# Kernel tuning notes

Hardware: AMD Instinct MI355X
Metric: run time of the kernel (lower is better)

Reference implementation:

```python
import jax, jax.numpy as jnp
import numpy as np

TEMPERATURE = 0.07
NEG_INF = -1e9
EPS = 1e-12  # matches F.normalize eps

B, N, D = 512, 128, 512


def _l2norm(x):
    return x / jnp.maximum(jnp.linalg.norm(x, axis=-1, keepdims=True), EPS)


def setup_inputs() -> dict:
    key = jax.random.key(0)
    k1, k2, k3, k4 = jax.random.split(key, 4)
    text_embeddings = jax.random.normal(k1, (B, D), dtype=jnp.float32)
    all_visual_embeddings = jax.random.normal(k2, (B, N, D), dtype=jnp.float32)
    valid = jax.random.bernoulli(k3, 0.9, (B, N))
    gt_indices = jax.random.randint(k4, (B,), 0, N, dtype=jnp.int64 if jax.config.jax_enable_x64 else jnp.int32)
    return {
        'text_embeddings': text_embeddings,
        'all_visual_embeddings': all_visual_embeddings,
        'valid': valid,
        'gt_indices': gt_indices,
    }


def reference(text_embeddings, all_visual_embeddings, valid, gt_indices):
    Bb, Nn, Dd = all_visual_embeddings.shape
    tn = _l2norm(text_embeddings)                 # (B, D)
    vn = _l2norm(all_visual_embeddings)           # (B, N, D)

    gt_c = jnp.clip(gt_indices, 0, Nn - 1)
    barange = jnp.arange(Bb)
    gt_vis = vn[barange, gt_c]                    # (B, D) GT visual per sample
    sample_valid = (gt_indices >= 0) & (gt_indices < Nn) & valid[barange, gt_c]  # (B,)

    pos_sim = jnp.sum(tn * gt_vis, axis=-1) / TEMPERATURE            # (B,)

    # in-sample hard negatives: all valid humans except GT
    sims_in = jnp.einsum('bd,bnd->bn', tn, vn) / TEMPERATURE          # (B, N)
    in_mask = valid & (jnp.arange(Nn)[None, :] != gt_c[:, None])      # (B, N)

    # in-batch negatives: other samples' valid GT visuals
    sims_batch = (tn @ gt_vis.T) / TEMPERATURE                        # (B, B)
    batch_mask = sample_valid[None, :] & ~jnp.eye(Bb, dtype=bool)     # (B, B)

    neg_logits = jnp.concatenate([
        jnp.where(in_mask, sims_in, NEG_INF),
        jnp.where(batch_mask, sims_batch, NEG_INF),
    ], axis=1)                                                        # (B, N+B)

    # CE with label 0 over [pos, negs] = logsumexp - pos
    lse = jax.nn.logsumexp(jnp.concatenate([pos_sim[:, None], neg_logits], axis=1), axis=1)
    loss_per = lse - pos_sim                                          # (B,)

    has_neg = jnp.any(in_mask, axis=1) | jnp.any(batch_mask, axis=1)
    contrib = sample_valid & has_neg
    n_valid = jnp.sum(sample_valid.astype(jnp.float32))
    denom = jnp.maximum(n_valid, 1.0)

    total = jnp.sum(jnp.where(contrib, loss_per, 0.0)) / denom
    max_neg = jnp.max(neg_logits, axis=1)
    correct = contrib & (pos_sim >= max_neg)  # argmax ties go to index 0 (pos)
    accuracy = jnp.sum(correct.astype(jnp.float32)) / denom
    return total, accuracy
```

## Files before the change

kernel.cpp:

```cpp
#include <hip/hip_runtime.h>
#include <hip/hip_bf16.h>
#include <math.h>

constexpr int B_ = 512;
constexpr int N_ = 128;
constexpr int D_ = 512;
constexpr float TEMP_INV = 1.0f / 0.07f;
constexpr float NEG_INF_ = -1e9f;
constexpr float EPS_ = 1e-12f;

constexpr size_t OFF_TN   = 0;
constexpr size_t OFF_GTV  = OFF_TN + (size_t)B_ * D_;
constexpr size_t OFF_POS  = OFF_GTV + (size_t)B_ * D_;
constexpr size_t OFF_LIN  = OFF_POS + B_;
constexpr size_t OFF_LB   = OFF_LIN + (size_t)B_ * N_;
constexpr size_t OFF_SV   = OFF_LB + (size_t)B_ * B_;
constexpr size_t OFF_SCAL = OFF_SV + B_;

__device__ __forceinline__ float wave_sum(float v) {
    for (int off = 32; off; off >>= 1) v += __shfl_xor(v, off);
    return v;
}

__device__ __forceinline__ void detect_flags(const void* raw, int lane, int& f0, int& f1) {
    unsigned int v = ((const unsigned int*)raw)[lane];
    f0 = (__ballot(v == 0x3f800000u) != 0ull) ? 1 : 0;
    f1 = (__ballot((v & 0xffffff00u) != 0u) != 0ull) ? 1 : 0;
}

__device__ __forceinline__ int decode_valid(const void* raw, int f0, int f1, size_t idx) {
    if (f0) return ((const float*)raw)[idx] != 0.0f;
    if (f1) return ((const unsigned char*)raw)[idx] != 0;
    return ((const int*)raw)[idx] != 0;
}

__global__ __launch_bounds__(256) void fused_insample_kernel(
        const float* __restrict__ text,
        const float* __restrict__ visual,
        const int* __restrict__ gt,
        const void* __restrict__ valid_raw,
        float* __restrict__ tn,
        float* __restrict__ gtv,
        float* __restrict__ pos_sim,
        int* __restrict__ svalid,
        float* __restrict__ scal,
        float* __restrict__ lin) {
    int bid = blockIdx.x;
    int b = bid >> 2;
    int tile = bid & 3;
    int tid = threadIdx.x;
    int wave = tid >> 6, lane = tid & 63;

    if (bid == 0 && tid < 3) scal[tid] = 0.0f;

    int f0, f1;
    detect_flags(valid_raw, lane, f0, f1);

    __shared__ float4 tsh4[D_ / 4];
    float* tshf = (float*)tsh4;
    const float* trow = text + (size_t)b * D_;
    float t0 = trow[tid], t1 = trow[tid + 256];
    float sst = wave_sum(t0 * t0 + t1 * t1);
    __shared__ float red[4];
    __shared__ float invt_sh;
    if (lane == 0) red[wave] = sst;
    __syncthreads();
    if (tid == 0) invt_sh = 1.0f / fmaxf(sqrtf(red[0] + red[1] + red[2] + red[3]), EPS_);
    __syncthreads();
    float invt = invt_sh;
    t0 *= invt; t1 *= invt;
    tshf[tid] = t0; tshf[tid + 256] = t1;
    if (tile == 0) {
        tn[(size_t)b * D_ + tid]       = t0;
        tn[(size_t)b * D_ + tid + 256] = t1;
    }
    __syncthreads();

    int g = gt[b];
    int gc = min(max(g, 0), N_ - 1);
    int sub = lane >> 4;
    int s = lane & 15;

    #pragma unroll
    for (int p = 0; p < 2; ++p) {
        int n = tile * 32 + p * 16 + wave * 4 + sub;
        const float4* vrow = (const float4*)(visual + ((size_t)b * N_ + n) * D_);
        float dot = 0.0f, ss = 0.0f;
        #pragma unroll
        for (int it = 0; it < 8; ++it) {
            float4 v = vrow[s + 16 * it];
            float4 t = tsh4[s + 16 * it];
            dot += v.x * t.x + v.y * t.y + v.z * t.z + v.w * t.w;
            ss  += v.x * v.x + v.y * v.y + v.z * v.z + v.w * v.w;
        }
        #pragma unroll
        for (int off = 8; off; off >>= 1) {
            dot += __shfl_xor(dot, off);
            ss  += __shfl_xor(ss, off);
        }
        float inv = 1.0f / fmaxf(sqrtf(ss), EPS_);
        if (s == 0) {
            int vb = decode_valid(valid_raw, f0, f1, (size_t)b * N_ + n);
            bool m = vb && (n != gc);
            lin[(size_t)b * N_ + n] = m ? dot * inv * TEMP_INV : NEG_INF_;
            if (n == gc) {
                pos_sim[b] = dot * inv * TEMP_INV;
                svalid[b] = (g >= 0 && g < N_ && vb) ? 1 : 0;
            }
        }
        if (n == gc) {
            float4* gdst = (float4*)(gtv + (size_t)b * D_);
            #pragma unroll
            for (int it = 0; it < 8; ++it) {
                float4 v = vrow[s + 16 * it];
                gdst[s + 16 * it] = make_float4(v.x * inv, v.y * inv, v.z * inv, v.w * inv);
            }
        }
    }
}

__global__ __launch_bounds__(256) void batch_kernel(const float* __restrict__ gtv,
                                                    const float* __restrict__ tn,
                                                    const int* __restrict__ svalid,
                                                    float* __restrict__ lb) {
    int bid = blockIdx.x;
    int b0 = (bid >> 2) * 4;
    int jbase = (bid & 3) * 128;
    int tid = threadIdx.x;
    __shared__ float4 tsh4[4 * (D_ / 4)];
    #pragma unroll
    for (int idx = tid; idx < 4 * (D_ / 4); idx += 256) {
        int r = idx >> 7, c = idx & 127;
        tsh4[idx] = ((const float4*)tn)[(size_t)(b0 + r) * (D_ / 4) + c];
    }
    __syncthreads();
    int wave = tid >> 6, lane = tid & 63;
    int sub = lane >> 4;
    int s = lane & 15;
    #pragma unroll
    for (int p = 0; p < 8; ++p) {
        int j = jbase + p * 16 + wave * 4 + sub;
        const float4* grow = (const float4*)gtv + (size_t)j * (D_ / 4);
        float a0 = 0.0f, a1 = 0.0f, a2 = 0.0f, a3 = 0.0f;
        #pragma unroll
        for (int it = 0; it < 8; ++it) {
            float4 v  = grow[s + 16 * it];
            float4 t0 = tsh4[0 * 128 + s + 16 * it];
            float4 t1 = tsh4[1 * 128 + s + 16 * it];
            float4 t2 = tsh4[2 * 128 + s + 16 * it];
            float4 t3 = tsh4[3 * 128 + s + 16 * it];
            a0 += v.x * t0.x + v.y * t0.y + v.z * t0.z + v.w * t0.w;
            a1 += v.x * t1.x + v.y * t1.y + v.z * t1.z + v.w * t1.w;
            a2 += v.x * t2.x + v.y * t2.y + v.z * t2.z + v.w * t2.w;
            a3 += v.x * t3.x + v.y * t3.y + v.z * t3.z + v.w * t3.w;
        }
        #pragma unroll
        for (int off = 8; off; off >>= 1) {
            a0 += __shfl_xor(a0, off);
            a1 += __shfl_xor(a1, off);
            a2 += __shfl_xor(a2, off);
            a3 += __shfl_xor(a3, off);
        }
        int sv = svalid[j];
        if (s < 4) {
            float av = (s == 0) ? a0 : (s == 1) ? a1 : (s == 2) ? a2 : a3;
            int brow = b0 + s;
            lb[(size_t)brow * B_ + j] = (sv && j != brow) ? av * TEMP_INV : NEG_INF_;
        }
    }
}

__global__ __launch_bounds__(256) void lse_kernel(const float* __restrict__ logits_in,
                                                  const float* __restrict__ lb,
                                                  const float* __restrict__ pos_sim,
                                                  const int* __restrict__ svalid,
                                                  float* __restrict__ accum,
                                                  int* __restrict__ done,
                                                  float* __restrict__ out) {
    int b = blockIdx.x;
    int tid = threadIdx.x;
    int wave = tid >> 6, lane = tid & 63;
    float pos = pos_sim[b];
    float x0 = (tid < N_) ? logits_in[(size_t)b * N_ + tid]
                          : lb[(size_t)b * B_ + (tid - N_)];
    float x1 = lb[(size_t)b * B_ + (tid + 256 - N_)];
    float x2 = (tid < N_) ? lb[(size_t)b * B_ + (tid + 512 - N_)] : NEG_INF_;
    float lmax = fmaxf(fmaxf(x0, x1), x2);
    for (int off = 32; off; off >>= 1) lmax = fmaxf(lmax, __shfl_xor(lmax, off));
    __shared__ float red[4];
    __shared__ float sh1;
    if (lane == 0) red[wave] = lmax;
    __syncthreads();
    if (tid == 0) sh1 = fmaxf(fmaxf(red[0], red[1]), fmaxf(red[2], red[3]));
    __syncthreads();
    float maxneg = sh1;
    float m = fmaxf(maxneg, pos);
    float lsum = __expf(x0 - m) + __expf(x1 - m) + ((tid < N_) ? __expf(x2 - m) : 0.0f);
    lsum = wave_sum(lsum);
    __syncthreads();
    if (lane == 0) red[wave] = lsum;
    __syncthreads();
    __shared__ int is_last;
    if (tid == 0) {
        float sum = red[0] + red[1] + red[2] + red[3] + __expf(pos - m);
        float lse = m + logf(sum);
        float loss = lse - pos;
        bool has_neg = maxneg > -1e8f;
        bool contrib = (svalid[b] != 0) && has_neg;
        if (contrib) {
            atomicAdd(&accum[0], loss);
            if (pos >= maxneg) atomicAdd(&accum[1], 1.0f);
        }
        __threadfence();
        int prev = atomicAdd(done, 1);
        is_last = (prev == B_ - 1) ? 1 : 0;
    }
    __syncthreads();
    if (is_last) {
        int v = svalid[tid] + svalid[tid + 256];
        for (int off = 32; off; off >>= 1) v += __shfl_xor(v, off);
        __shared__ int ired[4];
        if (lane == 0) ired[wave] = v;
        __syncthreads();
        if (tid == 0) {
            int nv = ired[0] + ired[1] + ired[2] + ired[3];
            float total = atomicAdd(&accum[0], 0.0f);
            float acc   = atomicAdd(&accum[1], 0.0f);
            float denom = fmaxf((float)nv, 1.0f);
            out[0] = total / denom;
            out[1] = acc / denom;
        }
    }
}

extern "C" void kernel_launch(void* const* d_in, const int* in_sizes, int n_in,
                              void* d_out, int out_size, void* d_ws, size_t ws_size,
                              hipStream_t stream) {
    const float* text   = (const float*)d_in[0];
    const float* visual = (const float*)d_in[1];
    const void*  valid  = d_in[2];
    const int*   gt     = (const int*)d_in[3];
    float* out = (float*)d_out;

    float* wsf = (float*)d_ws;
    float* tn      = wsf + OFF_TN;
    float* gtv     = wsf + OFF_GTV;
    float* pos_sim = wsf + OFF_POS;
    float* lin     = wsf + OFF_LIN;
    float* lb      = wsf + OFF_LB;
    int*   svalid  = (int*)(wsf + OFF_SV);
    float* scal    = wsf + OFF_SCAL;
    float* accum   = scal;
    int*   done    = (int*)(scal + 2);

    fused_insample_kernel<<<B_ * 4, 256, 0, stream>>>(text, visual, gt, valid,
                                                      tn, gtv, pos_sim, svalid, scal, lin);
    batch_kernel<<<B_, 256, 0, stream>>>(gtv, tn, svalid, lb);
    lse_kernel<<<B_, 256, 0, stream>>>(lin, lb, pos_sim, svalid, accum, done, out);
}
```

Baseline: 227.4 us.

## Fuse batch-similarity and logsumexp kernels, keep batch logits in shared memory

Merges batch_kernel and lse_kernel into one kernel. Each 512-thread block handles two text rows, computes their 512 in-batch logits into shared memory, then does the logsumexp and accumulation directly. This removes one launch and the round trip of the B×B logits buffer through global memory. The visual loads in the in-sample kernel also become nontemporal loads to reduce cache pollution. The trade-off is that each block now reads all of gtv for only two rows instead of four, which halves reuse of gtv per block and doubles its total reads.

```diff
diff --git a/kernel.cpp b/kernel.cpp
--- a/kernel.cpp
+++ b/kernel.cpp
@@ -1,5 +1,4 @@
 #include <hip/hip_runtime.h>
-#include <hip/hip_bf16.h>
 #include <math.h>
 
 constexpr int B_ = 512;
@@ -9,12 +8,13 @@
 constexpr float NEG_INF_ = -1e9f;
 constexpr float EPS_ = 1e-12f;
 
+typedef float f4v __attribute__((ext_vector_type(4)));
+
 constexpr size_t OFF_TN   = 0;
 constexpr size_t OFF_GTV  = OFF_TN + (size_t)B_ * D_;
 constexpr size_t OFF_POS  = OFF_GTV + (size_t)B_ * D_;
 constexpr size_t OFF_LIN  = OFF_POS + B_;
-constexpr size_t OFF_LB   = OFF_LIN + (size_t)B_ * N_;
-constexpr size_t OFF_SV   = OFF_LB + (size_t)B_ * B_;
+constexpr size_t OFF_SV   = OFF_LIN + (size_t)B_ * N_;
 constexpr size_t OFF_SCAL = OFF_SV + B_;
 
 __device__ __forceinline__ float wave_sum(float v) {
@@ -84,11 +84,11 @@
     #pragma unroll
     for (int p = 0; p < 2; ++p) {
         int n = tile * 32 + p * 16 + wave * 4 + sub;
-        const float4* vrow = (const float4*)(visual + ((size_t)b * N_ + n) * D_);
+        const f4v* vrow = (const f4v*)(visual + ((size_t)b * N_ + n) * D_);
         float dot = 0.0f, ss = 0.0f;
         #pragma unroll
         for (int it = 0; it < 8; ++it) {
-            float4 v = vrow[s + 16 * it];
+            f4v v = __builtin_nontemporal_load(vrow + s + 16 * it);
             float4 t = tsh4[s + 16 * it];
             dot += v.x * t.x + v.y * t.y + v.z * t.z + v.w * t.w;
             ss  += v.x * v.x + v.y * v.y + v.z * v.z + v.w * v.w;
@@ -109,100 +109,88 @@
             }
         }
         if (n == gc) {
-            float4* gdst = (float4*)(gtv + (size_t)b * D_);
+            f4v* gdst = (f4v*)(gtv + (size_t)b * D_);
             #pragma unroll
             for (int it = 0; it < 8; ++it) {
-                float4 v = vrow[s + 16 * it];
-                gdst[s + 16 * it] = make_float4(v.x * inv, v.y * inv, v.z * inv, v.w * inv);
+                f4v v = __builtin_nontemporal_load(vrow + s + 16 * it);
+                gdst[s + 16 * it] = v * inv;
             }
         }
     }
 }
 
-__global__ __launch_bounds__(256) void batch_kernel(const float* __restrict__ gtv,
-                                                    const float* __restrict__ tn,
-                                                    const int* __restrict__ svalid,
-                                                    float* __restrict__ lb) {
-    int bid = blockIdx.x;
-    int b0 = (bid >> 2) * 4;
-    int jbase = (bid & 3) * 128;
+__global__ __launch_bounds__(512) void batch_lse_kernel(
+        const float* __restrict__ gtv,
+        const float* __restrict__ tn,
+        const float* __restrict__ lin,
+        const float* __restrict__ pos_sim,
+        const int* __restrict__ svalid,
+        float* __restrict__ accum,
+        int* __restrict__ done,
+        float* __restrict__ out) {
+    int b0 = blockIdx.x * 2;
     int tid = threadIdx.x;
-    __shared__ float4 tsh4[4 * (D_ / 4)];
-    #pragma unroll
-    for (int idx = tid; idx < 4 * (D_ / 4); idx += 256) {
+    int wave = tid >> 6, lane = tid & 63;
+
+    __shared__ float4 tsh[2 * (D_ / 4)];
+    __shared__ float lbsh[2][B_];
+    for (int idx = tid; idx < 2 * (D_ / 4); idx += 512) {
         int r = idx >> 7, c = idx & 127;
-        tsh4[idx] = ((const float4*)tn)[(size_t)(b0 + r) * (D_ / 4) + c];
-    }
-    __syncthreads();
-    int wave = tid >> 6, lane = tid & 63;
-    int sub = lane >> 4;
-    int s = lane & 15;
-    #pragma unroll
-    for (int p = 0; p < 8; ++p) {
-        int j = jbase + p * 16 + wave * 4 + sub;
+        tsh[idx] = ((const float4*)tn)[(size_t)(b0 + r) * (D_ / 4) + c];
+    }
+    __syncthreads();
+
+    int q = tid >> 4;
+    int s = tid & 15;
+    #pragma unroll 4
+    for (int p = 0; p < 16; ++p) {
+        int j = p * 32 + q;
         const float4* grow = (const float4*)gtv + (size_t)j * (D_ / 4);
-        float a0 = 0.0f, a1 = 0.0f, a2 = 0.0f, a3 = 0.0f;
+        float a0 = 0.0f, a1 = 0.0f;
         #pragma unroll
         for (int it = 0; it < 8; ++it) {
             float4 v  = grow[s + 16 * it];
-            float4 t0 = tsh4[0 * 128 + s + 16 * it];
-            float4 t1 = tsh4[1 * 128 + s + 16 * it];
-            float4 t2 = tsh4[2 * 128 + s + 16 * it];
-            float4 t3 = tsh4[3 * 128 + s + 16 * it];
+            float4 t0 = tsh[0 * 128 + s + 16 * it];
+            float4 t1 = tsh[1 * 128 + s + 16 * it];
             a0 += v.x * t0.x + v.y * t0.y + v.z * t0.z + v.w * t0.w;
             a1 += v.x * t1.x + v.y * t1.y + v.z * t1.z + v.w * t1.w;
-            a2 += v.x * t2.x + v.y * t2.y + v.z * t2.z + v.w * t2.w;
-            a3 += v.x * t3.x + v.y * t3.y + v.z * t3.z + v.w * t3.w;
         }
         #pragma unroll
         for (int off = 8; off; off >>= 1) {
             a0 += __shfl_xor(a0, off);
             a1 += __shfl_xor(a1, off);
-            a2 += __shfl_xor(a2, off);
-            a3 += __shfl_xor(a3, off);
-        }
-        int sv = svalid[j];
-        if (s < 4) {
-            float av = (s == 0) ? a0 : (s == 1) ? a1 : (s == 2) ? a2 : a3;
+        }
+        if (s < 2) {
+            float av = (s == 0) ? a0 : a1;
             int brow = b0 + s;
-            lb[(size_t)brow * B_ + j] = (sv && j != brow) ? av * TEMP_INV : NEG_INF_;
-        }
-    }
-}
-
-__global__ __launch_bounds__(256) void lse_kernel(const float* __restrict__ logits_in,
-                                                  const float* __restrict__ lb,
-                                                  const float* __restrict__ pos_sim,
-                                                  const int* __restrict__ svalid,
-                                                  float* __restrict__ accum,
-                                                  int* __restrict__ done,
-                                                  float* __restrict__ out) {
-    int b = blockIdx.x;
-    int tid = threadIdx.x;
-    int wave = tid >> 6, lane = tid & 63;
+            lbsh[s][j] = (svalid[j] && j != brow) ? av * TEMP_INV : NEG_INF_;
+        }
+    }
+    __syncthreads();
+
+    int r = tid >> 8;
+    int rt = tid & 255;
+    int b = b0 + r;
     float pos = pos_sim[b];
-    float x0 = (tid < N_) ? logits_in[(size_t)b * N_ + tid]
-                          : lb[(size_t)b * B_ + (tid - N_)];
-    float x1 = lb[(size_t)b * B_ + (tid + 256 - N_)];
-    float x2 = (tid < N_) ? lb[(size_t)b * B_ + (tid + 512 - N_)] : NEG_INF_;
+    float x0 = (rt < N_) ? lin[(size_t)b * N_ + rt] : lbsh[r][rt - N_];
+    float x1 = lbsh[r][rt + 256 - N_];
+    float x2 = (rt < N_) ? lbsh[r][rt + 512 - N_] : NEG_INF_;
     float lmax = fmaxf(fmaxf(x0, x1), x2);
     for (int off = 32; off; off >>= 1) lmax = fmaxf(lmax, __shfl_xor(lmax, off));
-    __shared__ float red[4];
-    __shared__ float sh1;
-    if (lane == 0) red[wave] = lmax;
-    __syncthreads();
-    if (tid == 0) sh1 = fmaxf(fmaxf(red[0], red[1]), fmaxf(red[2], red[3]));
-    __syncthreads();
-    float maxneg = sh1;
+    __shared__ float redm[8], reds[8];
+    if (lane == 0) redm[wave] = lmax;
+    __syncthreads();
+    float maxneg = fmaxf(fmaxf(redm[r * 4 + 0], redm[r * 4 + 1]),
+                         fmaxf(redm[r * 4 + 2], redm[r * 4 + 3]));
     float m = fmaxf(maxneg, pos);
-    float lsum = __expf(x0 - m) + __expf(x1 - m) + ((tid < N_) ? __expf(x2 - m) : 0.0f);
+    float lsum = __expf(x0 - m) + __expf(x1 - m) + ((rt < N_) ? __expf(x2 - m) : 0.0f);
     lsum = wave_sum(lsum);
-    __syncthreads();
-    if (lane == 0) red[wave] = lsum;
+    if (lane == 0) reds[wave] = lsum;
     __syncthreads();
     __shared__ int is_last;
-    if (tid == 0) {
-        float sum = red[0] + red[1] + red[2] + red[3] + __expf(pos - m);
+    if (rt == 0) {
+        float sum = reds[r * 4 + 0] + reds[r * 4 + 1] + reds[r * 4 + 2] + reds[r * 4 + 3]
+                  + __expf(pos - m);
         float lse = m + logf(sum);
         float loss = lse - pos;
         bool has_neg = maxneg > -1e8f;
@@ -212,18 +200,23 @@
             if (pos >= maxneg) atomicAdd(&accum[1], 1.0f);
         }
         __threadfence();
+    }
+    __syncthreads();
+    if (tid == 0) {
         int prev = atomicAdd(done, 1);
-        is_last = (prev == B_ - 1) ? 1 : 0;
+        is_last = (prev == (int)gridDim.x - 1) ? 1 : 0;
     }
     __syncthreads();
     if (is_last) {
-        int v = svalid[tid] + svalid[tid + 256];
+        int v = svalid[tid];
         for (int off = 32; off; off >>= 1) v += __shfl_xor(v, off);
-        __shared__ int ired[4];
+        __shared__ int ired[8];
         if (lane == 0) ired[wave] = v;
         __syncthreads();
         if (tid == 0) {
-            int nv = ired[0] + ired[1] + ired[2] + ired[3];
+            int nv = 0;
+            #pragma unroll
+            for (int w = 0; w < 8; ++w) nv += ired[w];
             float total = atomicAdd(&accum[0], 0.0f);
             float acc   = atomicAdd(&accum[1], 0.0f);
             float denom = fmaxf((float)nv, 1.0f);
@@ -247,7 +240,6 @@
     float* gtv     = wsf + OFF_GTV;
     float* pos_sim = wsf + OFF_POS;
     float* lin     = wsf + OFF_LIN;
-    float* lb      = wsf + OFF_LB;
     int*   svalid  = (int*)(wsf + OFF_SV);
     float* scal    = wsf + OFF_SCAL;
     float* accum   = scal;
@@ -255,6 +247,6 @@
 
     fused_insample_kernel<<<B_ * 4, 256, 0, stream>>>(text, visual, gt, valid,
                                                       tn, gtv, pos_sim, svalid, scal, lin);
-    batch_kernel<<<B_, 256, 0, stream>>>(gtv, tn, svalid, lb);
-    lse_kernel<<<B_, 256, 0, stream>>>(lin, lb, pos_sim, svalid, accum, done, out);
-}
+    batch_lse_kernel<<<B_ / 2, 512, 0, stream>>>(gtv, tn, lin, pos_sim, svalid,
+                                                 accum, done, out);
+}
```

Result: faster. 215.1 us (-5.4%).
